# Kernel optimization log

Hardware: AMD Instinct MI355X
Metric: run time of the kernel (lower is better)

## Reference

```python
import jax, jax.numpy as jnp
import numpy as np

N_SIGMA = 1
K_INST = 8  # instance ids 1..K_INST (0 = background)
W_INST, W_VAR, W_SEED = 1.0, 10.0, 1.0
FG_WEIGHT = 1.0


def make_xym(h, w):
    # torch buffer: linspace(0,2,2048) x / linspace(0,1,1024) y, sliced to [0:h,0:w]
    xm = jnp.linspace(0.0, 2.0, 2048)[:w]
    ym = jnp.linspace(0.0, 1.0, 1024)[:h]
    return jnp.stack([jnp.broadcast_to(xm[None, :], (h, w)),
                      jnp.broadcast_to(ym[:, None], (h, w))], axis=0)  # [2,h,w]


def lovasz_hinge_flat(logits, labels):
    # logits, labels: [N] float (labels in {0,1})
    signs = 2.0 * labels - 1.0
    errors = 1.0 - logits * signs
    order = jnp.argsort(-errors)            # descending sort of errors
    errors_sorted = errors[order]
    gt_sorted = labels[order]
    gts = gt_sorted.sum()
    inter = gts - jnp.cumsum(gt_sorted)
    union = gts + jnp.cumsum(1.0 - gt_sorted)
    jac = 1.0 - inter / union
    grad = jnp.concatenate([jac[:1], jac[1:] - jac[:-1]])
    # torch impl wraps grad in Variable() -> no gradient through grad
    return jnp.dot(jax.nn.relu(errors_sorted), jax.lax.stop_gradient(grad))


def spatial_emb_loss(predictions, instances):
    B, C, T, h, w = predictions.shape
    xym = make_xym(h, w)
    # Faithful to the torch source: due to loop indentation, only the last
    # time step's var/instance/seed losses survive, and obj_count == 1.
    pred = predictions[:, :, T - 1]          # [B,C,h,w]
    inst = instances[:, 0, T - 1]            # [B,h,w] int
    spatial_emb = jnp.tanh(pred[:, 0:2]) + xym[None]   # [B,2,h,w]
    sigma = pred[:, 2:2 + N_SIGMA]                     # [B,1,h,w]
    seed = jax.nn.sigmoid(pred[:, 2 + N_SIGMA])        # [B,h,w]
    npix = float(h * w)

    def per_image(se, sig, sd, ins):
        bg_loss = jnp.sum(jnp.where(ins == 0, sd ** 2, 0.0))

        def per_id(k):
            m = (ins == k).astype(se.dtype)            # [h,w]
            cnt = m.sum()
            safe = jnp.maximum(cnt, 1.0)
            # to_center=True: center of in-mask pixel coordinates
            center = jnp.sum(xym * m[None], axis=(1, 2)) / safe      # [2]
            s_mean = jnp.sum(sig * m[None], axis=(1, 2)) / safe      # [n_sigma]
            var_l = jnp.sum(m[None] * (sig - jax.lax.stop_gradient(s_mean)[:, None, None]) ** 2) / (safe * N_SIGMA)
            s_exp = jnp.exp(s_mean * 10.0)
            dist = jnp.exp(-jnp.sum((se - center[:, None, None]) ** 2 * s_exp[:, None, None], axis=0))  # [h,w]
            inst_l = lovasz_hinge_flat((dist * 2.0 - 1.0).reshape(-1), m.reshape(-1))
            seed_l = FG_WEIGHT * jnp.sum(m * (sd - jax.lax.stop_gradient(dist)) ** 2)
            present = (cnt > 0).astype(se.dtype)       # torch skips absent ids
            return present * var_l, present * inst_l, present * seed_l

        var_l, inst_l, seed_l = jax.vmap(per_id)(jnp.arange(1, K_INST + 1))
        seed_loss = (bg_loss + seed_l.sum()) / npix
        # obj_count == 1 in the original code (incremented once per t-loop)
        return W_INST * inst_l.sum() + W_VAR * var_l.sum() + W_SEED * seed_loss

    per_b = jax.vmap(per_image)(spatial_emb, sigma, seed, inst)
    # torch: loss = loss / b, with b == B-1 after the loop
    return per_b.sum() / (B - 1)


def setup_inputs():
    key = jax.random.key(0)
    k1, k2 = jax.random.split(key)
    B, C, T, H, W = 4, 4, 2, 512, 1024
    predictions = jax.random.normal(k1, (B, C, T, H, W), dtype=jnp.float32)
    instances = jax.random.randint(k2, (B, 1, T, H, W), 0, K_INST + 1, dtype=jnp.int32)
    labels = jnp.zeros((B, 1, T, H, W), dtype=jnp.int32)  # unused by forward
    return {"predictions": predictions, "instances": instances, "labels": labels}


def reference(predictions, instances, labels):
    return spatial_emb_loss(predictions, instances)
```

## Files before the change

### kernel.cpp

```cpp
#include <hip/hip_runtime.h>

#define H 512
#define WID 1024
#define HW (H*WID)
#define B 4
#define K 8
#define NB 1024
#define NBLK1 128

#define OFF_LOSS  0
#define OFF_TICK  1
#define OFF_FIN   16
#define OFF_SPART 512
#define OFF_PART  (OFF_SPART + B*K*NBLK1*8)

static __device__ __forceinline__ float frcp(float x){
#if __has_builtin(__builtin_amdgcn_rcpf)
  return __builtin_amdgcn_rcpf(x);
#else
  return 1.0f / x;
#endif
}
static __device__ __forceinline__ float fexp2(float x){
#if __has_builtin(__builtin_amdgcn_exp2f)
  return __builtin_amdgcn_exp2f(x);
#else
  return exp2f(x);
#endif
}
static __device__ __forceinline__ float ftanh(float x){
  return 1.0f - 2.0f * frcp(__expf(2.0f*x) + 1.0f);
}
static __device__ __forceinline__ float fsigmoid(float x){
  return frcp(1.0f + __expf(-x));
}

__global__ __launch_bounds__(512) void k1_stats(const float* __restrict__ pred,
                                                const int* __restrict__ inst,
                                                float* __restrict__ ws) {
  const int b = blockIdx.y;
  __shared__ int4   ti[1024];
  __shared__ float4 ts[1024];
  __shared__ float  part5[K][5];
  if (b == 0 && blockIdx.x == 0) {
    if (threadIdx.x == 0) ws[OFF_LOSS] = 0.0f;
    if (threadIdx.x == 1) ((unsigned int*)ws)[OFF_TICK] = 0u;
  }
  const float4* sig4 = (const float4*)(pred + (size_t)(8*b + 5) * HW);
  const int4*   ins4 = (const int4*)(inst + (size_t)(2*b + 1) * HW);
  const int base4 = blockIdx.x * 1024;
  #pragma unroll
  for (int i = 0; i < 2; i++) {
    const int q = threadIdx.x + i*512;
    ti[q] = ins4[base4 + q];
    ts[q] = sig4[base4 + q];
  }
  __syncthreads();
  const int wv = threadIdx.x >> 6, lane = threadIdx.x & 63;
  const int kk = wv + 1;
  float cnt=0.f, sx=0.f, sy=0.f, ss=0.f, ss2=0.f;
  #pragma unroll
  for (int j = 0; j < 16; j++) {
    const int q = lane + 64*j;
    const int4   iv = ti[q];
    const float4 sv = ts[q];
    const int p = (base4 + q) * 4;
    const float xm0 = (float)(p & (WID-1)) * (2.0f/2047.0f);
    const float ym  = (float)(p >> 10)     * (1.0f/1023.0f);
    const float m0 = (iv.x==kk)?1.f:0.f, m1=(iv.y==kk)?1.f:0.f,
                m2 = (iv.z==kk)?1.f:0.f, m3=(iv.w==kk)?1.f:0.f;
    const float msum = (m0+m1)+(m2+m3);
    cnt += msum;
    sx  += msum*xm0 + (m1 + 2.0f*m2 + 3.0f*m3)*(2.0f/2047.0f);
    sy  += msum*ym;
    ss  += m0*sv.x + m1*sv.y + m2*sv.z + m3*sv.w;
    ss2 += m0*sv.x*sv.x + m1*sv.y*sv.y + m2*sv.z*sv.z + m3*sv.w*sv.w;
  }
  #pragma unroll
  for (int o=1;o<64;o<<=1){
    cnt+=__shfl_xor(cnt,o,64);
    sx +=__shfl_xor(sx, o,64);
    sy +=__shfl_xor(sy, o,64);
    ss +=__shfl_xor(ss, o,64);
    ss2+=__shfl_xor(ss2,o,64);
  }
  if (lane == 0) {
    part5[wv][0]=cnt; part5[wv][1]=sx; part5[wv][2]=sy; part5[wv][3]=ss; part5[wv][4]=ss2;
  }
  __syncthreads();
  if (threadIdx.x < K*8) {
    const int w = threadIdx.x >> 3, c = threadIdx.x & 7;
    if (c < 5)
      ws[OFF_SPART + ((size_t)(b*K + w)*NBLK1 + blockIdx.x)*8 + c] = part5[w][c];
  }
}

template<int G>
__global__ __launch_bounds__(1024, 8) void k3_main(const float* __restrict__ pred,
                                                   const int* __restrict__ inst,
                                                   float* __restrict__ ws,
                                                   unsigned int* __restrict__ part) {
  const int b = blockIdx.y, g = blockIdx.x;
  __shared__ unsigned int hist[K*NB];
  __shared__ float4 finL[K];
  __shared__ float  vlocL[K];
  for (int i = threadIdx.x*4; i < K*NB; i += 1024*4)
    *(uint4*)&hist[i] = make_uint4(0u,0u,0u,0u);
  const int wv = threadIdx.x >> 6, lane = threadIdx.x & 63;
  if (wv < K) {
    const float* p = ws + OFF_SPART + (size_t)(b*K + wv)*NBLK1*8;
    const float4 q0 = *(const float4*)(p + (size_t)lane*8);
    const float  e0 = p[(size_t)lane*8 + 4];
    const float4 q1 = *(const float4*)(p + (size_t)(lane+64)*8);
    const float  e1 = p[(size_t)(lane+64)*8 + 4];
    float a0=q0.x+q1.x, a1=q0.y+q1.y, a2=q0.z+q1.z, a3=q0.w+q1.w, a4=e0+e1;
    #pragma unroll
    for (int o=1;o<64;o<<=1){
      a0+=__shfl_xor(a0,o,64); a1+=__shfl_xor(a1,o,64); a2+=__shfl_xor(a2,o,64);
      a3+=__shfl_xor(a3,o,64); a4+=__shfl_xor(a4,o,64);
    }
    if (lane == 0) {
      const float cnt=a0, sx=a1, sy=a2, ss=a3, ss2=a4;
      const float present = (cnt > 0.0f) ? 1.0f : 0.0f;
      const float safe = fmaxf(cnt, 1.0f);
      const float cx = sx/safe, cy = sy/safe, sm = ss/safe;
      const float var = (ss2 - 2.0f*sm*ss + sm*sm*cnt)/safe;
      const float sexp = expf(10.0f * sm);
      const float L2E = 1.4426950408889634f;
      finL[wv] = make_float4(-sexp*L2E,
                              2.0f*sexp*cx*L2E,
                              2.0f*sexp*cy*L2E,
                             -sexp*(cx*cx + cy*cy)*L2E + 10.0f);
      vlocL[wv] = present * 10.0f * var * (1.0f/3.0f);
      if (g == 0) ws[OFF_FIN + (b*K + wv)*8 + 4] = cnt;
    }
  }
  __syncthreads();
  float4 fr[K];
  #pragma unroll
  for (int k=0;k<K;k++) fr[k] = finL[k];
  const float4* p0 = (const float4*)(pred + (size_t)(8*b+1)*HW);
  const float4* p1 = (const float4*)(pred + (size_t)(8*b+3)*HW);
  const float4* p3 = (const float4*)(pred + (size_t)(8*b+7)*HW);
  const int4*   in4 = (const int4*)(inst + (size_t)(2*b+1)*HW);
  float sAcc = 0.0f;
  constexpr int CH4 = HW / (G*4);
  const int base4 = g * CH4;
  for (int q0 = 0; q0 < CH4; q0 += 1024) {
    const int idx = base4 + q0 + threadIdx.x;
    const int4   iv = in4[idx];
    const float4 f0 = p0[idx];
    const float4 f1 = p1[idx];
    const float4 f3 = p3[idx];
    const int p = idx * 4;
    const float xm0 = (float)(p & (WID-1)) * (2.0f/2047.0f);
    const float ym  = (float)(p >> 10)     * (1.0f/1023.0f);
    const int ivv[4] = {iv.x, iv.y, iv.z, iv.w};
    float pxv[4], pyv[4], t2v[4], down[4];
    {
      const float a0v[4] = {f0.x, f0.y, f0.z, f0.w};
      const float a1v[4] = {f1.x, f1.y, f1.z, f1.w};
      #pragma unroll
      for (int e=0;e<4;e++){
        pxv[e] = ftanh(a0v[e]) + xm0 + (float)e*(2.0f/2047.0f);
        pyv[e] = ftanh(a1v[e]) + ym;
        t2v[e] = pxv[e]*pxv[e] + pyv[e]*pyv[e];
        down[e] = 0.0f;
      }
    }
    #pragma unroll
    for (int j=0;j<K;j++){
      const float4 f = fr[j];
      int buv[4]; unsigned addv[4];
      #pragma unroll
      for (int e=0;e<4;e++){
        const float u = fmaf(f.x, t2v[e], fmaf(f.y, pxv[e], fmaf(f.z, pyv[e], f.w)));
        const float v = fexp2(u);
        int vi = (int)v; vi = (vi > NB-1) ? NB-1 : vi;
        const bool own = (ivv[e] == j+1);
        if (own) down[e] = v;
        buv[e] = own ? (NB-1 - vi) : vi;
        addv[e] = own ? 0x10001u : 1u;
      }
      int cur = buv[0]; unsigned acc = addv[0];
      #pragma unroll
      for (int e=1;e<4;e++){
        const bool same = (buv[e] == cur);
        if (!same) atomicAdd(&hist[j*NB + cur], acc);
        acc = same ? acc + addv[e] : addv[e];
        cur = buv[e];
      }
      atomicAdd(&hist[j*NB + cur], acc);
    }
    {
      const float sdv[4] = {fsigmoid(f3.x), fsigmoid(f3.y), fsigmoid(f3.z), fsigmoid(f3.w)};
      #pragma unroll
      for (int e=0;e<4;e++){
        const float d  = (ivv[e] == 0) ? 0.0f : down[e] * (1.0f/1024.0f);
        const float df = sdv[e] - d;
        sAcc += df*df;
      }
    }
  }
  __syncthreads();
  unsigned int* dst = part + ((size_t)b*G + g)*(K*NB);
  for (int i = threadIdx.x*4; i < K*NB; i += 1024*4)
    *(uint4*)&dst[i] = *(const uint4*)&hist[i];
  #pragma unroll
  for (int o=1;o<64;o<<=1) sAcc += __shfl_xor(sAcc, o, 64);
  __shared__ float wsum[16];
  if (lane == 0) wsum[wv] = sAcc;
  __syncthreads();
  if (threadIdx.x == 0) {
    float tot = 0.f;
    #pragma unroll
    for (int w = 0; w < 16; w++) tot += wsum[w];
    float add = tot * (1.0f/((float)HW * 3.0f));
    if (g == 0) {
      #pragma unroll
      for (int k = 0; k < K; k++) add += vlocL[k];
    }
    atomicAdd(ws + OFF_LOSS, add);
  }
}

__global__ __launch_bounds__(1024) void k4ab_lovasz(const unsigned int* __restrict__ part,
                                                    float* __restrict__ ws,
                                                    float* __restrict__ out, int G_) {
  const int bk = blockIdx.x;
  const int b = bk >> 3, k = bk & 7;
  const int t = threadIdx.x, lane = t & 63, wv = t >> 6;
  __shared__ int    wtc[16], wtp[16];
  __shared__ double racc[16];
  const float cntF = ws[OFF_FIN + bk*8 + 4];
  if (cntF > 0.0f) {
    const double Pd = (double)cntF;
    const int bu = NB-1 - t;
    unsigned rc = 0, rp = 0;
    const unsigned int* base = part + (size_t)b*G_*(K*NB) + (size_t)k*NB + bu;
    #pragma unroll 8
    for (int g = 0; g < G_; g++) {
      const unsigned v = base[(size_t)g*(K*NB)];
      rc += v & 0xFFFFu;
      rp += v >> 16;
    }
    int ic = (int)rc, ip = (int)rp;
    #pragma unroll
    for (int o=1;o<64;o<<=1){
      const int vc = __shfl_up(ic, o, 64);
      const int vp = __shfl_up(ip, o, 64);
      if (lane >= o) { ic += vc; ip += vp; }
    }
    if (lane == 63) { wtc[wv] = ic; wtp[wv] = ip; }
    __syncthreads();
    int offc = 0, offp = 0;
    for (int w = 0; w < wv; w++) { offc += wtc[w]; offp += wtp[w]; }
    const int irun = offc + ic - (int)rc;
    const int crun = offp + ip - (int)rp;
    double acc = 0.0;
    if (rc) {
      const double jac0 = (irun==0) ? 0.0 : 1.0 - (Pd - crun)/(Pd + irun - crun);
      const int ir1 = irun + (int)rc, cr1 = crun + (int)rp;
      const double jac1 = 1.0 - (Pd - cr1)/(Pd + ir1 - cr1);
      acc = ((bu + 0.5) * (2.0/NB)) * (jac1 - jac0);
    }
    #pragma unroll
    for (int o=1;o<64;o<<=1) acc += __shfl_xor(acc, o, 64);
    if (lane == 0) racc[wv] = acc;
    __syncthreads();
    if (t == 0) {
      double tot = 0.0;
      #pragma unroll
      for (int w = 0; w < 16; w++) tot += racc[w];
      atomicAdd(ws + OFF_LOSS, (float)(tot * (1.0/3.0)));
    }
  }
  if (t == 0) {
    __threadfence();
    unsigned int* wsu = (unsigned int*)ws;
    const unsigned int old = atomicAdd(&wsu[OFF_TICK], 1u);
    if (old == (unsigned)(B*K - 1)) {
      __threadfence();
      out[0] = *((volatile float*)(ws + OFF_LOSS));
    }
  }
}

extern "C" void kernel_launch(void* const* d_in, const int* in_sizes, int n_in,
                              void* d_out, int out_size, void* d_ws, size_t ws_size,
                              hipStream_t stream) {
  const float* pred = (const float*)d_in[0];
  const int*   inst = (const int*)d_in[1];
  float* ws  = (float*)d_ws;
  float* out = (float*)d_out;
  unsigned int* part = ((unsigned int*)d_ws) + OFF_PART;
  int G = 128;
  while (G > 32 && ws_size < ((size_t)OFF_PART + (size_t)B*G*K*NB)*4) G >>= 1;
  k1_stats<<<dim3(NBLK1,B), 512, 0, stream>>>(pred, inst, ws);
  if      (G == 128) k3_main<128><<<dim3(128,B), 1024, 0, stream>>>(pred, inst, ws, part);
  else if (G ==  64) k3_main< 64><<<dim3( 64,B), 1024, 0, stream>>>(pred, inst, ws, part);
  else               k3_main< 32><<<dim3( 32,B), 1024, 0, stream>>>(pred, inst, ws, part);
  k4ab_lovasz<<<B*K, 1024, 0, stream>>>(part, ws, out, G);
}
```

Measured before the change: 133.4 us.

## Split Lovasz histogram reduction across more blocks with atomic merge and last-block finish

The final kernel now runs 8 blocks per (image, instance) instead of 1. Each block reduces one 128-bin chunk of the per-block histograms across all G partial groups and atomically adds the result into a zeroed global buffer. A per-(b,k) ticket counter picks the last-arriving block, which then does the prefix scan and Jaccard accumulation from the merged histogram. The goal is to spread the serial G-deep gather over more CUs. The cost is extra atomics, an extra workspace region that k1 must zero, and a last-block handoff that depends on fences being correct.

```diff
diff --git a/kernel.cpp b/kernel.cpp
--- a/kernel.cpp
+++ b/kernel.cpp
@@ -10,9 +10,11 @@
 
 #define OFF_LOSS  0
 #define OFF_TICK  1
-#define OFF_FIN   16
+#define OFF_TICK2 2
+#define OFF_FIN   64
 #define OFF_SPART 512
-#define OFF_PART  (OFF_SPART + B*K*NBLK1*8)
+#define OFF_RED   (OFF_SPART + B*K*NBLK1*8)
+#define OFF_PART  (OFF_RED + 2*B*K*NB)
 
 static __device__ __forceinline__ float frcp(float x){
 #if __has_builtin(__builtin_amdgcn_rcpf)
@@ -37,14 +39,18 @@
 
 __global__ __launch_bounds__(512) void k1_stats(const float* __restrict__ pred,
                                                 const int* __restrict__ inst,
-                                                float* __restrict__ ws) {
+                                                float* __restrict__ ws,
+                                                unsigned int* __restrict__ red) {
   const int b = blockIdx.y;
   __shared__ int4   ti[1024];
   __shared__ float4 ts[1024];
   __shared__ float  part5[K][5];
-  if (b == 0 && blockIdx.x == 0) {
-    if (threadIdx.x == 0) ws[OFF_LOSS] = 0.0f;
-    if (threadIdx.x == 1) ((unsigned int*)ws)[OFF_TICK] = 0u;
+  {
+    const int blin = b*NBLK1 + blockIdx.x;
+    if (threadIdx.x < 32)
+      ((uint4*)red)[(size_t)blin*32 + threadIdx.x] = make_uint4(0u,0u,0u,0u);
+    if (blin == 0 && threadIdx.x >= 32 && threadIdx.x < 66)
+      ((unsigned int*)ws)[threadIdx.x - 32] = 0u;
   }
   const float4* sig4 = (const float4*)(pred + (size_t)(8*b + 5) * HW);
   const int4*   ins4 = (const int4*)(inst + (size_t)(2*b + 1) * HW);
@@ -224,26 +230,53 @@
   }
 }
 
-__global__ __launch_bounds__(1024) void k4ab_lovasz(const unsigned int* __restrict__ part,
-                                                    float* __restrict__ ws,
-                                                    float* __restrict__ out, int G_) {
-  const int bk = blockIdx.x;
+__global__ __launch_bounds__(1024) void k4_red(const unsigned int* __restrict__ part,
+                                               float* __restrict__ ws,
+                                               unsigned int* __restrict__ red,
+                                               float* __restrict__ out, int G_) {
+  const int bid = blockIdx.x;
+  const int bk = bid >> 3, chunk = bid & 7;
   const int b = bk >> 3, k = bk & 7;
   const int t = threadIdx.x, lane = t & 63, wv = t >> 6;
+  __shared__ unsigned int cnt2[1024], pos2[1024];
   __shared__ int    wtc[16], wtp[16];
   __shared__ double racc[16];
+  __shared__ unsigned int lastFlag;
+  {
+    const int gg = t >> 7, bl = t & 127;
+    const int bu = chunk*128 + bl;
+    unsigned rc = 0, rp = 0;
+    #pragma unroll 4
+    for (int g = gg; g < G_; g += 8) {
+      const unsigned v = part[((size_t)(b*G_ + g)*K + k)*NB + bu];
+      rc += v & 0xFFFFu;
+      rp += v >> 16;
+    }
+    cnt2[t] = rc; pos2[t] = rp;
+  }
+  __syncthreads();
+  if (t < 128) {
+    unsigned c = 0, p = 0;
+    #pragma unroll
+    for (int q = 0; q < 8; q++) { c += cnt2[q*128 + t]; p += pos2[q*128 + t]; }
+    const int bu = chunk*128 + t;
+    if (c) atomicAdd(&red[(size_t)bk*NB + bu], c);
+    if (p) atomicAdd(&red[(size_t)B*K*NB + bk*NB + bu], p);
+  }
+  __syncthreads();
+  if (t == 0) {
+    __threadfence();
+    lastFlag = atomicAdd(&((unsigned int*)ws)[OFF_TICK2 + bk], 1u);
+  }
+  __syncthreads();
+  if (lastFlag != 7u) return;
+  __threadfence();
   const float cntF = ws[OFF_FIN + bk*8 + 4];
   if (cntF > 0.0f) {
     const double Pd = (double)cntF;
     const int bu = NB-1 - t;
-    unsigned rc = 0, rp = 0;
-    const unsigned int* base = part + (size_t)b*G_*(K*NB) + (size_t)k*NB + bu;
-    #pragma unroll 8
-    for (int g = 0; g < G_; g++) {
-      const unsigned v = base[(size_t)g*(K*NB)];
-      rc += v & 0xFFFFu;
-      rp += v >> 16;
-    }
+    const unsigned rc = red[(size_t)bk*NB + bu];
+    const unsigned rp = red[(size_t)B*K*NB + bk*NB + bu];
     int ic = (int)rc, ip = (int)rp;
     #pragma unroll
     for (int o=1;o<64;o<<=1){
@@ -293,12 +326,13 @@
   const int*   inst = (const int*)d_in[1];
   float* ws  = (float*)d_ws;
   float* out = (float*)d_out;
+  unsigned int* red  = ((unsigned int*)d_ws) + OFF_RED;
   unsigned int* part = ((unsigned int*)d_ws) + OFF_PART;
   int G = 128;
   while (G > 32 && ws_size < ((size_t)OFF_PART + (size_t)B*G*K*NB)*4) G >>= 1;
-  k1_stats<<<dim3(NBLK1,B), 512, 0, stream>>>(pred, inst, ws);
+  k1_stats<<<dim3(NBLK1,B), 512, 0, stream>>>(pred, inst, ws, red);
   if      (G == 128) k3_main<128><<<dim3(128,B), 1024, 0, stream>>>(pred, inst, ws, part);
   else if (G ==  64) k3_main< 64><<<dim3( 64,B), 1024, 0, stream>>>(pred, inst, ws, part);
   else               k3_main< 32><<<dim3( 32,B), 1024, 0, stream>>>(pred, inst, ws, part);
-  k4ab_lovasz<<<B*K, 1024, 0, stream>>>(part, ws, out, G);
-}
+  k4_red<<<B*K*8, 1024, 0, stream>>>(part, ws, red, out, G);
+}
```

Result: slower. 147.1 us (+10.3%).
